# Optimization experiments

Hardware: AMD Instinct MI355X
Metric: run time of the kernel (lower is better)

The kernel has to match this reference:

```python
import jax, jax.numpy as jnp
import numpy as np

V_CNT = 10000
B = 16
N = B * V_CNT          # total nodes
K = 6                  # Chebyshev order
CH = [3, 128, 64, 32, 128]
G = 8                  # GroupNorm groups (divides 128, 64, 32)
EPS = 1e-5
AVG_DEG = 16


def setup_inputs() -> dict:
    key = jax.random.key(0)
    ks = jax.random.split(key, 8)
    n_edges = N * AVG_DEG
    inp = {
        "x": jax.random.normal(ks[0], (N, CH[0]), jnp.float32),
        "edge_index": jax.random.randint(ks[1], (2, n_edges), 0, N, jnp.int32).astype(jnp.int64),
    }
    for l in range(3):
        cin, cout = CH[l], CH[l + 1]
        s = (1.0 / (cin * K)) ** 0.5
        inp[f"W{l}"] = jax.random.uniform(ks[2 + l], (K, cin, cout), jnp.float32, -s, s)
        inp[f"b{l}"] = jnp.zeros((cout,), jnp.float32)
        inp[f"gamma{l}"] = jnp.ones((cout,), jnp.float32)
        inp[f"beta{l}"] = jnp.zeros((cout,), jnp.float32)
    din = V_CNT * CH[3]
    s = (1.0 / din) ** 0.5
    inp["W_last"] = jax.random.uniform(ks[5], (din, CH[4]), jnp.float32, -s, s)
    inp["b_last"] = jnp.zeros((CH[4],), jnp.float32)
    return inp


def _cheb_edge_weights(edge_index):
    # PyG ChebConv sym normalization with lambda_max=2: L_hat = L - I = -D^{-1/2} A D^{-1/2}
    row, col = edge_index[0], edge_index[1]
    deg = jax.ops.segment_sum(jnp.ones(row.shape, jnp.float32), row, num_segments=N)
    dis = jnp.where(deg > 0, jax.lax.rsqrt(jnp.maximum(deg, 1.0)), 0.0)  # deg^{-1/2}, inf->0
    return -dis[row] * dis[col], row, col


def _cheb_conv(x, row, col, w, W, b):
    # Chebyshev recursion: Tx0=x, Tx1=L_hat x, Tx_k = 2 L_hat Tx_{k-1} - Tx_{k-2}
    prop = lambda h: jax.ops.segment_sum(w[:, None] * h[col], row, num_segments=N)
    Tx0 = x
    out = Tx0 @ W[0]
    Tx1 = prop(Tx0)
    out = out + Tx1 @ W[1]
    for k in range(2, W.shape[0]):
        Tx2 = 2.0 * prop(Tx1) - Tx0
        out = out + Tx2 @ W[k]
        Tx0, Tx1 = Tx1, Tx2
    return out + b


def _group_norm(h, gamma, beta):
    n, C = h.shape
    hg = h.reshape(n, G, C // G)
    mu = hg.mean(axis=2, keepdims=True)
    var = hg.var(axis=2, keepdims=True)
    hg = (hg - mu) * jax.lax.rsqrt(var + EPS)
    return hg.reshape(n, C) * gamma + beta


def reference(x, edge_index, W0, b0, gamma0, beta0, W1, b1, gamma1, beta1,
              W2, b2, gamma2, beta2, W_last, b_last):
    w, row, col = _cheb_edge_weights(edge_index)
    Ws = [W0, W1, W2]
    bs = [b0, b1, b2]
    gs = [gamma0, gamma1, gamma2]
    betas = [beta0, beta1, beta2]
    h = x
    for l in range(3):
        h = _cheb_conv(h, row, col, w, Ws[l], bs[l])
        h = _group_norm(h, gs[l], betas[l])
        h = jax.nn.relu(h)
    h = h.reshape(-1, V_CNT * CH[3])  # [B, v_cnt*32]
    return h @ W_last + b_last
```

## Files before the change

### kernel.cpp

```cpp
#include <hip/hip_runtime.h>
#include <hip/hip_fp16.h>


#define NN 160000
#define EE 2560000
#define FD2 256
#define NBKT 625
#define BCAPL 13
#define ABLK 500
#define EPT 20

typedef __attribute__((ext_vector_type(8))) _Float16 half8;
typedef __attribute__((ext_vector_type(4))) float floatx4;

__device__ inline float2 h2f2(unsigned u) {
  __half2 h = __builtin_bit_cast(__half2, u);
  return __half22float2(h);
}
__device__ inline unsigned short f2h(float f) {
  return __builtin_bit_cast(unsigned short, __float2half_rn(f));
}
__device__ inline unsigned packh2(float a, float b) {
  return __builtin_bit_cast(unsigned, __floats2half2_rn(a, b));
}

__global__ __launch_bounds__(256) void k_binit(int* __restrict__ bcur) {
  int i = blockIdx.x * 256 + threadIdx.x;
  if (i < NBKT) bcur[i] = i << BCAPL;
}

__global__ __launch_bounds__(256) void k_bucketA(const int* __restrict__ ei,
                                                 int* __restrict__ bcur, unsigned* __restrict__ stg) {
  __shared__ int bcnt[NBKT];
  __shared__ int gbase[NBKT];
  int tid = threadIdx.x;
  for (int i = tid; i < NBKT; i += 256) bcnt[i] = 0;
  __syncthreads();
  int r[EPT];
  int e0 = blockIdx.x * (256 * EPT);
#pragma unroll
  for (int k = 0; k < EPT; k++) {
    int e = e0 + k * 256 + tid;
    r[k] = ei[e];
    atomicAdd(&bcnt[r[k] >> 8], 1);
  }
  __syncthreads();
  for (int i = tid; i < NBKT; i += 256) {
    gbase[i] = atomicAdd(&bcur[i], bcnt[i]);
    bcnt[i] = 0;
  }
  __syncthreads();
#pragma unroll
  for (int k = 0; k < EPT; k++) {
    int e = e0 + k * 256 + tid;
    int c = ei[EE + e];
    int b = r[k] >> 8;
    int off = atomicAdd(&bcnt[b], 1);
    int pos = gbase[b] + off;
    if (pos < ((b + 1) << BCAPL))
      stg[pos] = ((unsigned)(r[k] & 255) << 18) | (unsigned)c;
  }
}

__global__ void k_bktscan(const int* __restrict__ bcur, int* __restrict__ bbase,
                          int* __restrict__ rowStart) {
  __shared__ int s[1024];
  int tid = threadIdx.x;
  int tot = 0;
  if (tid < NBKT) {
    tot = bcur[tid] - (tid << BCAPL);
    if (tot > (1 << BCAPL)) tot = 1 << BCAPL;
  }
  s[tid] = tot;
  __syncthreads();
  for (int off = 1; off < 1024; off <<= 1) {
    int t = (tid >= off) ? s[tid - off] : 0;
    __syncthreads();
    s[tid] += t;
    __syncthreads();
  }
  if (tid < NBKT) bbase[tid] = s[tid] - tot;
  if (tid == 0) rowStart[NN] = EE;
}

__global__ __launch_bounds__(256) void k_bucketB1(const unsigned* __restrict__ stg, const int* __restrict__ bcur,
                                                  const int* __restrict__ bbase, int* __restrict__ rowStart,
                                                  float* __restrict__ dis) {
  __shared__ int degl[256];
  __shared__ int s[256];
  int b = blockIdx.x;
  int tid = threadIdx.x;
  degl[tid] = 0;
  __syncthreads();
  int cnt = bcur[b] - (b << BCAPL);
  if (cnt > (1 << BCAPL)) cnt = 1 << BCAPL;
  int base = b << BCAPL;
  for (int k = tid; k < cnt; k += 256)
    atomicAdd(&degl[stg[base + k] >> 18], 1);
  __syncthreads();
  int d = degl[tid];
  s[tid] = d;
  __syncthreads();
  for (int off = 1; off < 256; off <<= 1) {
    int t = (tid >= off) ? s[tid - off] : 0;
    __syncthreads();
    s[tid] += t;
    __syncthreads();
  }
  int r0 = b << 8;
  rowStart[r0 + tid] = bbase[b] + s[tid] - d;
  dis[r0 + tid] = d > 0 ? rsqrtf((float)d) : 0.f;
}

__global__ __launch_bounds__(256) void k_bucketB2(const unsigned* __restrict__ stg, const int* __restrict__ bcur,
                                                  const int* __restrict__ rowStart, const float* __restrict__ dis,
                                                  int2* __restrict__ ew) {
  __shared__ int curs[256];
  __shared__ float disl[256];
  int b = blockIdx.x;
  int tid = threadIdx.x;
  int r0 = b << 8;
  curs[tid] = rowStart[r0 + tid];
  disl[tid] = dis[r0 + tid];
  __syncthreads();
  int cnt = bcur[b] - (b << BCAPL);
  if (cnt > (1 << BCAPL)) cnt = 1 << BCAPL;
  int base = b << BCAPL;
  for (int k = tid; k < cnt; k += 256) {
    unsigned u = stg[base + k];
    int rlow = u >> 18;
    int c = u & 0x3FFFFu;
    int pos = atomicAdd(&curs[rlow], 1);
    float w = -disl[rlow] * dis[c];
    ew[pos] = make_int2(c, __float_as_int(w));
  }
}

__global__ __launch_bounds__(256) void k_copyx(const float* __restrict__ x, float* __restrict__ A,
                                               unsigned short* __restrict__ TxAll) {
  int i = blockIdx.x * 256 + threadIdx.x;
  if (i >= NN) return;
  float v0 = x[i * 3], v1 = x[i * 3 + 1], v2 = x[i * 3 + 2];
  A[i * 3] = v0; A[i * 3 + 1] = v1; A[i * 3 + 2] = v2;
  uint4* dst = reinterpret_cast<uint4*>(TxAll + (size_t)i * 32);
  uint4 z = make_uint4(0u, 0u, 0u, 0u);
  dst[0] = make_uint4(packh2(v0, v1), (unsigned)f2h(v2), 0u, 0u);
  dst[1] = z; dst[2] = z; dst[3] = z;
}

template <int MODE>
__global__ __launch_bounds__(256) void k_prop3(const float* __restrict__ Tsrc, float* __restrict__ Tdst,
                                               unsigned short* __restrict__ TxAll, int ks,
                                               const int* __restrict__ rowStart, const int2* __restrict__ ew) {
  int i = blockIdx.x * 256 + threadIdx.x;
  if (i >= NN) return;
  float a0 = 0.f, a1 = 0.f, a2 = 0.f;
  int e = rowStart[i], e1 = rowStart[i + 1];
  for (; e + 3 < e1; e += 4) {
    int2 p0 = ew[e], p1 = ew[e + 1], p2 = ew[e + 2], p3 = ew[e + 3];
    float w0 = __int_as_float(p0.y), w1 = __int_as_float(p1.y);
    float w2 = __int_as_float(p2.y), w3 = __int_as_float(p3.y);
    a0 += w0 * Tsrc[p0.x * 3] + w1 * Tsrc[p1.x * 3] + w2 * Tsrc[p2.x * 3] + w3 * Tsrc[p3.x * 3];
    a1 += w0 * Tsrc[p0.x * 3 + 1] + w1 * Tsrc[p1.x * 3 + 1] + w2 * Tsrc[p2.x * 3 + 1] + w3 * Tsrc[p3.x * 3 + 1];
    a2 += w0 * Tsrc[p0.x * 3 + 2] + w1 * Tsrc[p1.x * 3 + 2] + w2 * Tsrc[p2.x * 3 + 2] + w3 * Tsrc[p3.x * 3 + 2];
  }
  for (; e < e1; e++) {
    int2 p0 = ew[e];
    float w0 = __int_as_float(p0.y);
    a0 += w0 * Tsrc[p0.x * 3];
    a1 += w0 * Tsrc[p0.x * 3 + 1];
    a2 += w0 * Tsrc[p0.x * 3 + 2];
  }
  if (MODE == 2) {
    a0 = 2.f * a0 - Tdst[i * 3];
    a1 = 2.f * a1 - Tdst[i * 3 + 1];
    a2 = 2.f * a2 - Tdst[i * 3 + 2];
  }
  Tdst[i * 3] = a0; Tdst[i * 3 + 1] = a1; Tdst[i * 3 + 2] = a2;
  unsigned short* tp = TxAll + i * 32 + ks * 3;
  tp[0] = f2h(a0); tp[1] = f2h(a1); tp[2] = f2h(a2);
}

__global__ __launch_bounds__(256) void k_padW0(const float* __restrict__ W0, unsigned short* __restrict__ Bt) {
  int idx = blockIdx.x * 256 + threadIdx.x;
  if (idx >= 128 * 32) return;
  int co = idx >> 5, t = idx & 31;
  Bt[co * 32 + t] = (t < 18) ? f2h(W0[t * 128 + co]) : (unsigned short)0;
}

template <int CIN, int COUT>
__global__ __launch_bounds__(256) void k_combine(const float* __restrict__ W, unsigned short* __restrict__ Bt) {
  int idx = blockIdx.x * 256 + threadIdx.x;
  if (idx >= CIN * 6 * COUT) return;
  int co = idx % COUT;
  int j  = (idx / COUT) % 6;
  int ci = idx / (6 * COUT);
  float c0, c1, c2, c3, c4, c5;
  switch (j) {
    case 0:  c0 = 1;  c1 = 0;  c2 = -1; c3 = 0;   c4 = 1;  c5 = 0;   break;
    case 1:  c0 = 0;  c1 = 1;  c2 = 0;  c3 = -3;  c4 = 0;  c5 = 5;   break;
    case 2:  c0 = 0;  c1 = 0;  c2 = 2;  c3 = 0;   c4 = -8; c5 = 0;   break;
    case 3:  c0 = 0;  c1 = 0;  c2 = 0;  c3 = 4;   c4 = 0;  c5 = -20; break;
    case 4:  c0 = 0;  c1 = 0;  c2 = 0;  c3 = 0;   c4 = 8;  c5 = 0;   break;
    default: c0 = 0;  c1 = 0;  c2 = 0;  c3 = 0;   c4 = 0;  c5 = 16;  break;
  }
  float s = 0.f;
  s += c0 * W[(0 * CIN + ci) * COUT + co];
  s += c1 * W[(1 * CIN + ci) * COUT + co];
  s += c2 * W[(2 * CIN + ci) * COUT + co];
  s += c3 * W[(3 * CIN + ci) * COUT + co];
  s += c4 * W[(4 * CIN + ci) * COUT + co];
  s += c5 * W[(5 * CIN + ci) * COUT + co];
  Bt[(j * COUT + co) * CIN + ci] = f2h(s);
}

template <int KDIM, int COUT>
__global__ __launch_bounds__(256) void k_gemm(const unsigned short* __restrict__ A,
                                              const unsigned short* __restrict__ Bt,
                                              unsigned short* __restrict__ Y) {
  constexpr int KP = KDIM + 8;
  __shared__ unsigned short As[64 * KP];
  __shared__ unsigned short Bs[64 * KP];
  int i0 = blockIdx.x * 64;
  int c0 = blockIdx.y * 64;
  for (int idx = threadIdx.x; idx < 64 * (KDIM / 8); idx += 256) {
    int row = idx / (KDIM / 8), seg = idx % (KDIM / 8);
    uint4 v = ((const uint4*)A)[(size_t)(i0 + row) * (KDIM / 8) + seg];
    *reinterpret_cast<uint4*>(&As[row * KP + seg * 8]) = v;
  }
  for (int idx = threadIdx.x; idx < 64 * (KDIM / 8); idx += 256) {
    int row = idx / (KDIM / 8), seg = idx % (KDIM / 8);
    uint4 v = ((const uint4*)Bt)[(size_t)(c0 + row) * (KDIM / 8) + seg];
    *reinterpret_cast<uint4*>(&Bs[row * KP + seg * 8]) = v;
  }
  __syncthreads();
  int w = threadIdx.x >> 6, lane = threadIdx.x & 63;
  int mn = lane & 15, q = lane >> 4;
  floatx4 acc[4];
#pragma unroll
  for (int cb = 0; cb < 4; cb++) acc[cb] = {0.f, 0.f, 0.f, 0.f};
#pragma unroll
  for (int ks = 0; ks < KDIM / 32; ks++) {
    half8 af = *reinterpret_cast<const half8*>(&As[(16 * w + mn) * KP + ks * 32 + q * 8]);
#pragma unroll
    for (int cb = 0; cb < 4; cb++) {
      half8 bf = *reinterpret_cast<const half8*>(&Bs[(cb * 16 + mn) * KP + ks * 32 + q * 8]);
      acc[cb] = __builtin_amdgcn_mfma_f32_16x16x32_f16(af, bf, acc[cb], 0, 0, 0);
    }
  }
#pragma unroll
  for (int cb = 0; cb < 4; cb++) {
    int jc = c0 + cb * 16 + mn;
    int slice = jc / COUT, cc = jc % COUT;
    unsigned short* dst = Y + (size_t)slice * NN * COUT + cc;
#pragma unroll
    for (int r = 0; r < 4; r++) {
      int i = i0 + 16 * w + q * 4 + r;
      dst[(size_t)i * COUT] = f2h(acc[cb][r]);
    }
  }
}

template <int CPN>
__global__ __launch_bounds__(256) void k_horner(const unsigned* __restrict__ Ysrc, unsigned* __restrict__ Ydst,
                                                const int* __restrict__ rowStart, const int2* __restrict__ ew) {
  int t = blockIdx.x * 256 + threadIdx.x;
  int i = t / CPN;
  int cp = t % CPN;
  float2 a = h2f2(Ydst[(size_t)i * CPN + cp]);
  float acc0 = a.x, acc1 = a.y;
  int e = rowStart[i], e1 = rowStart[i + 1];
  for (; e + 7 < e1; e += 8) {
    int2 p[8];
    unsigned u[8];
#pragma unroll
    for (int k = 0; k < 8; k++) p[k] = ew[e + k];
#pragma unroll
    for (int k = 0; k < 8; k++) u[k] = Ysrc[(size_t)p[k].x * CPN + cp];
#pragma unroll
    for (int k = 0; k < 8; k++) {
      float w = __int_as_float(p[k].y);
      float2 f = h2f2(u[k]);
      acc0 += w * f.x;
      acc1 += w * f.y;
    }
  }
  for (; e < e1; e++) {
    int2 p0 = ew[e];
    float w0 = __int_as_float(p0.y);
    float2 f0 = h2f2(Ysrc[(size_t)p0.x * CPN + cp]);
    acc0 += w0 * f0.x;
    acc1 += w0 * f0.y;
  }
  Ydst[(size_t)i * CPN + cp] = packh2(acc0, acc1);
}

template <int CPG>
__global__ __launch_bounds__(256) void k_gn(const unsigned short* __restrict__ src, const float* __restrict__ bias,
                                            const float* __restrict__ gamma, const float* __restrict__ beta,
                                            unsigned short* __restrict__ dst) {
  constexpr int C = CPG * 8;
  int t = blockIdx.x * 256 + threadIdx.x;
  int i = t >> 3, g = t & 7;
  float v[CPG];
  const unsigned* p = reinterpret_cast<const unsigned*>(src + (size_t)i * C + g * CPG);
#pragma unroll
  for (int q = 0; q < CPG / 2; q++) {
    float2 f = h2f2(p[q]);
    v[2 * q] = f.x; v[2 * q + 1] = f.y;
  }
  float mean = 0.f;
#pragma unroll
  for (int c = 0; c < CPG; c++) { v[c] += bias[g * CPG + c]; mean += v[c]; }
  mean *= (1.f / CPG);
  float var = 0.f;
#pragma unroll
  for (int c = 0; c < CPG; c++) { float d = v[c] - mean; var += d * d; }
  var *= (1.f / CPG);
  float rs = rsqrtf(var + 1e-5f);
  unsigned* dp = reinterpret_cast<unsigned*>(dst + (size_t)i * C + g * CPG);
#pragma unroll
  for (int q = 0; q < CPG / 2; q++) {
    float o0 = fmaxf((v[2 * q] - mean) * rs * gamma[g * CPG + 2 * q] + beta[g * CPG + 2 * q], 0.f);
    float o1 = fmaxf((v[2 * q + 1] - mean) * rs * gamma[g * CPG + 2 * q + 1] + beta[g * CPG + 2 * q + 1], 0.f);
    dp[q] = packh2(o0, o1);
  }
}

__global__ __launch_bounds__(256) void k_final1(const unsigned short* __restrict__ h3,
                                                const float* __restrict__ Wl,
                                                float* __restrict__ part) {
  __shared__ float hs[16 * FD2];
  __shared__ float red[2048];
  int d0 = blockIdx.x * FD2;
  const unsigned* h3u = reinterpret_cast<const unsigned*>(h3);
  for (int idx = threadIdx.x; idx < 16 * (FD2 / 2); idx += 256) {
    int b = idx / (FD2 / 2), dq = idx % (FD2 / 2);
    float2 f = h2f2(h3u[(size_t)b * 160000 + (d0 >> 1) + dq]);
    hs[b * FD2 + 2 * dq] = f.x;
    hs[b * FD2 + 2 * dq + 1] = f.y;
  }
  __syncthreads();
  int w = threadIdx.x >> 6, lane = threadIdx.x & 63;
  float a0[16], a1[16];
#pragma unroll
  for (int b = 0; b < 16; b++) { a0[b] = 0.f; a1[b] = 0.f; }
  const float* wp = Wl + (size_t)(d0 + w * (FD2 / 4)) * 128 + 2 * lane;
#pragma unroll 2
  for (int r = 0; r < FD2 / 4; r++) {
    float2 wv = *reinterpret_cast<const float2*>(wp + (size_t)r * 128);
    int row = w * (FD2 / 4) + r;
#pragma unroll
    for (int b = 0; b < 16; b++) {
      float h = hs[b * FD2 + row];
      a0[b] += wv.x * h;
      a1[b] += wv.y * h;
    }
  }
  float2* red2 = reinterpret_cast<float2*>(red);
  for (int ww = 0; ww < 4; ww++) {
    if (w == ww) {
#pragma unroll
      for (int b = 0; b < 16; b++) {
        if (ww == 0) {
          red2[b * 64 + lane] = make_float2(a0[b], a1[b]);
        } else {
          float2 r2 = red2[b * 64 + lane];
          r2.x += a0[b]; r2.y += a1[b];
          red2[b * 64 + lane] = r2;
        }
      }
    }
    __syncthreads();
  }
  for (int i = threadIdx.x; i < 2048; i += 256)
    part[(size_t)blockIdx.x * 2048 + i] = red[i];
}

__global__ __launch_bounds__(256) void k_final2(const float* __restrict__ part, const float* __restrict__ bl,
                                                float* __restrict__ out) {
  int o = blockIdx.x * 256 + threadIdx.x;
  float s = bl[o & 127];
#pragma unroll 10
  for (int p = 0; p < 1250; p++) s += part[(size_t)p * 2048 + o];
  out[o] = s;
}

extern "C" void kernel_launch(void* const* d_in, const int* in_sizes, int n_in,
                              void* d_out, int out_size, void* d_ws, size_t ws_size,
                              hipStream_t stream) {
  const float* x   = (const float*)d_in[0];
  const int*   ei  = (const int*)d_in[1];
  const float* W0  = (const float*)d_in[2];
  const float* b0  = (const float*)d_in[3];
  const float* g0  = (const float*)d_in[4];
  const float* be0 = (const float*)d_in[5];
  const float* W1  = (const float*)d_in[6];
  const float* b1  = (const float*)d_in[7];
  const float* g1  = (const float*)d_in[8];
  const float* be1 = (const float*)d_in[9];
  const float* W2  = (const float*)d_in[10];
  const float* b2  = (const float*)d_in[11];
  const float* g2  = (const float*)d_in[12];
  const float* be2 = (const float*)d_in[13];
  const float* Wl  = (const float*)d_in[14];
  const float* bl  = (const float*)d_in[15];
  float* out = (float*)d_out;
  (void)in_sizes; (void)n_in; (void)out_size; (void)ws_size;

  char* pw = (char*)d_ws;
  auto carve = [&](size_t bytes) -> void* {
    void* r = (void*)pw;
    pw += (bytes + 255) & ~(size_t)255;
    return r;
  };
  int*            bcur     = (int*)   carve((size_t)NBKT * 4);
  int*            bbase    = (int*)   carve((size_t)NBKT * 4);
  int*            rowStart = (int*)   carve((size_t)(NN + 1) * 4);
  float*          dis      = (float*) carve((size_t)NN * 4);
  int2*           ew       = (int2*)  carve((size_t)EE * 8);
  unsigned short* Cwt      = (unsigned short*)carve((size_t)384 * 128 * 2);
  unsigned short* TxAll    = (unsigned short*)carve((size_t)NN * 32 * 2);
  float*          A3       = (float*) carve((size_t)NN * 3 * 4);
  float*          B3       = (float*) carve((size_t)NN * 3 * 4);
  unsigned short* Hbuf     = (unsigned short*)carve((size_t)NN * 128 * 2);
  unsigned short* Ybuf     = (unsigned short*)carve((size_t)NN * 384 * 2);
  float*          part     = (float*) carve((size_t)1250 * 2048 * 4);
  unsigned*       stg      = (unsigned*)Ybuf;

  k_binit<<<3, 256, 0, stream>>>(bcur);
  k_bucketA<<<ABLK, 256, 0, stream>>>(ei, bcur, stg);
  k_bktscan<<<1, 1024, 0, stream>>>(bcur, bbase, rowStart);
  k_bucketB1<<<NBKT, 256, 0, stream>>>(stg, bcur, bbase, rowStart, dis);
  k_bucketB2<<<NBKT, 256, 0, stream>>>(stg, bcur, rowStart, dis, ew);

  k_copyx<<<625, 256, 0, stream>>>(x, A3, TxAll);
  k_prop3<1><<<625, 256, 0, stream>>>(A3, B3, TxAll, 1, rowStart, ew);
  k_prop3<2><<<625, 256, 0, stream>>>(B3, A3, TxAll, 2, rowStart, ew);
  k_prop3<2><<<625, 256, 0, stream>>>(A3, B3, TxAll, 3, rowStart, ew);
  k_prop3<2><<<625, 256, 0, stream>>>(B3, A3, TxAll, 4, rowStart, ew);
  k_prop3<2><<<625, 256, 0, stream>>>(A3, B3, TxAll, 5, rowStart, ew);
  k_padW0<<<16, 256, 0, stream>>>(W0, Cwt);
  k_gemm<32, 128><<<dim3(2500, 2), 256, 0, stream>>>(TxAll, Cwt, Ybuf);
  k_gn<16><<<5000, 256, 0, stream>>>(Ybuf, b0, g0, be0, Hbuf);

  k_combine<128, 64><<<192, 256, 0, stream>>>(W1, Cwt);
  k_gemm<128, 64><<<dim3(2500, 6), 256, 0, stream>>>(Hbuf, Cwt, Ybuf);
  for (int j = 4; j >= 0; j--)
    k_horner<32><<<20000, 256, 0, stream>>>((unsigned*)(Ybuf + (size_t)(j + 1) * NN * 64),
                                            (unsigned*)(Ybuf + (size_t)j * NN * 64), rowStart, ew);
  k_gn<8><<<5000, 256, 0, stream>>>(Ybuf, b1, g1, be1, Hbuf);

  k_combine<64, 32><<<48, 256, 0, stream>>>(W2, Cwt);
  k_gemm<64, 32><<<dim3(2500, 3), 256, 0, stream>>>(Hbuf, Cwt, Ybuf);
  for (int j = 4; j >= 0; j--)
    k_horner<16><<<10000, 256, 0, stream>>>((unsigned*)(Ybuf + (size_t)(j + 1) * NN * 32),
                                            (unsigned*)(Ybuf + (size_t)j * NN * 32), rowStart, ew);
  k_gn<4><<<5000, 256, 0, stream>>>(Ybuf, b2, g2, be2, Hbuf);

  k_final1<<<1250, 256, 0, stream>>>(Hbuf, Wl, part);
  k_final2<<<8, 256, 0, stream>>>(part, bl, out);
}
```

Baseline: 1.281 ms.

## Fuse prep kernels, compress edge records, fuse GEMM/Horner with GroupNorm

Merges bucket init, weight combining/padding and x copy into one prep kernel, and folds the bucket scan into bucketB1 via a per-block reduction. Edge records shrink from 8-byte (col, weight) pairs to 4-byte words packing column and neighbour degree, with the weight rebuilt by rsqrt on the fly and the row-side scale applied once per node. The layer-0 GEMM now applies bias, GroupNorm and ReLU in its epilogue, and the last Horner step of layers 1 and 2 does the same, removing the separate GN passes. The aim is fewer launches and less gather traffic. The cost is extra rsqrt work per edge and degrees clamped to 8191.

```diff
diff --git a/kernel.cpp b/kernel.cpp
--- a/kernel.cpp
+++ b/kernel.cpp
@@ -24,174 +24,8 @@
   return __builtin_bit_cast(unsigned, __floats2half2_rn(a, b));
 }
 
-__global__ __launch_bounds__(256) void k_binit(int* __restrict__ bcur) {
-  int i = blockIdx.x * 256 + threadIdx.x;
-  if (i < NBKT) bcur[i] = i << BCAPL;
-}
-
-__global__ __launch_bounds__(256) void k_bucketA(const int* __restrict__ ei,
-                                                 int* __restrict__ bcur, unsigned* __restrict__ stg) {
-  __shared__ int bcnt[NBKT];
-  __shared__ int gbase[NBKT];
-  int tid = threadIdx.x;
-  for (int i = tid; i < NBKT; i += 256) bcnt[i] = 0;
-  __syncthreads();
-  int r[EPT];
-  int e0 = blockIdx.x * (256 * EPT);
-#pragma unroll
-  for (int k = 0; k < EPT; k++) {
-    int e = e0 + k * 256 + tid;
-    r[k] = ei[e];
-    atomicAdd(&bcnt[r[k] >> 8], 1);
-  }
-  __syncthreads();
-  for (int i = tid; i < NBKT; i += 256) {
-    gbase[i] = atomicAdd(&bcur[i], bcnt[i]);
-    bcnt[i] = 0;
-  }
-  __syncthreads();
-#pragma unroll
-  for (int k = 0; k < EPT; k++) {
-    int e = e0 + k * 256 + tid;
-    int c = ei[EE + e];
-    int b = r[k] >> 8;
-    int off = atomicAdd(&bcnt[b], 1);
-    int pos = gbase[b] + off;
-    if (pos < ((b + 1) << BCAPL))
-      stg[pos] = ((unsigned)(r[k] & 255) << 18) | (unsigned)c;
-  }
-}
-
-__global__ void k_bktscan(const int* __restrict__ bcur, int* __restrict__ bbase,
-                          int* __restrict__ rowStart) {
-  __shared__ int s[1024];
-  int tid = threadIdx.x;
-  int tot = 0;
-  if (tid < NBKT) {
-    tot = bcur[tid] - (tid << BCAPL);
-    if (tot > (1 << BCAPL)) tot = 1 << BCAPL;
-  }
-  s[tid] = tot;
-  __syncthreads();
-  for (int off = 1; off < 1024; off <<= 1) {
-    int t = (tid >= off) ? s[tid - off] : 0;
-    __syncthreads();
-    s[tid] += t;
-    __syncthreads();
-  }
-  if (tid < NBKT) bbase[tid] = s[tid] - tot;
-  if (tid == 0) rowStart[NN] = EE;
-}
-
-__global__ __launch_bounds__(256) void k_bucketB1(const unsigned* __restrict__ stg, const int* __restrict__ bcur,
-                                                  const int* __restrict__ bbase, int* __restrict__ rowStart,
-                                                  float* __restrict__ dis) {
-  __shared__ int degl[256];
-  __shared__ int s[256];
-  int b = blockIdx.x;
-  int tid = threadIdx.x;
-  degl[tid] = 0;
-  __syncthreads();
-  int cnt = bcur[b] - (b << BCAPL);
-  if (cnt > (1 << BCAPL)) cnt = 1 << BCAPL;
-  int base = b << BCAPL;
-  for (int k = tid; k < cnt; k += 256)
-    atomicAdd(&degl[stg[base + k] >> 18], 1);
-  __syncthreads();
-  int d = degl[tid];
-  s[tid] = d;
-  __syncthreads();
-  for (int off = 1; off < 256; off <<= 1) {
-    int t = (tid >= off) ? s[tid - off] : 0;
-    __syncthreads();
-    s[tid] += t;
-    __syncthreads();
-  }
-  int r0 = b << 8;
-  rowStart[r0 + tid] = bbase[b] + s[tid] - d;
-  dis[r0 + tid] = d > 0 ? rsqrtf((float)d) : 0.f;
-}
-
-__global__ __launch_bounds__(256) void k_bucketB2(const unsigned* __restrict__ stg, const int* __restrict__ bcur,
-                                                  const int* __restrict__ rowStart, const float* __restrict__ dis,
-                                                  int2* __restrict__ ew) {
-  __shared__ int curs[256];
-  __shared__ float disl[256];
-  int b = blockIdx.x;
-  int tid = threadIdx.x;
-  int r0 = b << 8;
-  curs[tid] = rowStart[r0 + tid];
-  disl[tid] = dis[r0 + tid];
-  __syncthreads();
-  int cnt = bcur[b] - (b << BCAPL);
-  if (cnt > (1 << BCAPL)) cnt = 1 << BCAPL;
-  int base = b << BCAPL;
-  for (int k = tid; k < cnt; k += 256) {
-    unsigned u = stg[base + k];
-    int rlow = u >> 18;
-    int c = u & 0x3FFFFu;
-    int pos = atomicAdd(&curs[rlow], 1);
-    float w = -disl[rlow] * dis[c];
-    ew[pos] = make_int2(c, __float_as_int(w));
-  }
-}
-
-__global__ __launch_bounds__(256) void k_copyx(const float* __restrict__ x, float* __restrict__ A,
-                                               unsigned short* __restrict__ TxAll) {
-  int i = blockIdx.x * 256 + threadIdx.x;
-  if (i >= NN) return;
-  float v0 = x[i * 3], v1 = x[i * 3 + 1], v2 = x[i * 3 + 2];
-  A[i * 3] = v0; A[i * 3 + 1] = v1; A[i * 3 + 2] = v2;
-  uint4* dst = reinterpret_cast<uint4*>(TxAll + (size_t)i * 32);
-  uint4 z = make_uint4(0u, 0u, 0u, 0u);
-  dst[0] = make_uint4(packh2(v0, v1), (unsigned)f2h(v2), 0u, 0u);
-  dst[1] = z; dst[2] = z; dst[3] = z;
-}
-
-template <int MODE>
-__global__ __launch_bounds__(256) void k_prop3(const float* __restrict__ Tsrc, float* __restrict__ Tdst,
-                                               unsigned short* __restrict__ TxAll, int ks,
-                                               const int* __restrict__ rowStart, const int2* __restrict__ ew) {
-  int i = blockIdx.x * 256 + threadIdx.x;
-  if (i >= NN) return;
-  float a0 = 0.f, a1 = 0.f, a2 = 0.f;
-  int e = rowStart[i], e1 = rowStart[i + 1];
-  for (; e + 3 < e1; e += 4) {
-    int2 p0 = ew[e], p1 = ew[e + 1], p2 = ew[e + 2], p3 = ew[e + 3];
-    float w0 = __int_as_float(p0.y), w1 = __int_as_float(p1.y);
-    float w2 = __int_as_float(p2.y), w3 = __int_as_float(p3.y);
-    a0 += w0 * Tsrc[p0.x * 3] + w1 * Tsrc[p1.x * 3] + w2 * Tsrc[p2.x * 3] + w3 * Tsrc[p3.x * 3];
-    a1 += w0 * Tsrc[p0.x * 3 + 1] + w1 * Tsrc[p1.x * 3 + 1] + w2 * Tsrc[p2.x * 3 + 1] + w3 * Tsrc[p3.x * 3 + 1];
-    a2 += w0 * Tsrc[p0.x * 3 + 2] + w1 * Tsrc[p1.x * 3 + 2] + w2 * Tsrc[p2.x * 3 + 2] + w3 * Tsrc[p3.x * 3 + 2];
-  }
-  for (; e < e1; e++) {
-    int2 p0 = ew[e];
-    float w0 = __int_as_float(p0.y);
-    a0 += w0 * Tsrc[p0.x * 3];
-    a1 += w0 * Tsrc[p0.x * 3 + 1];
-    a2 += w0 * Tsrc[p0.x * 3 + 2];
-  }
-  if (MODE == 2) {
-    a0 = 2.f * a0 - Tdst[i * 3];
-    a1 = 2.f * a1 - Tdst[i * 3 + 1];
-    a2 = 2.f * a2 - Tdst[i * 3 + 2];
-  }
-  Tdst[i * 3] = a0; Tdst[i * 3 + 1] = a1; Tdst[i * 3 + 2] = a2;
-  unsigned short* tp = TxAll + i * 32 + ks * 3;
-  tp[0] = f2h(a0); tp[1] = f2h(a1); tp[2] = f2h(a2);
-}
-
-__global__ __launch_bounds__(256) void k_padW0(const float* __restrict__ W0, unsigned short* __restrict__ Bt) {
-  int idx = blockIdx.x * 256 + threadIdx.x;
-  if (idx >= 128 * 32) return;
-  int co = idx >> 5, t = idx & 31;
-  Bt[co * 32 + t] = (t < 18) ? f2h(W0[t * 128 + co]) : (unsigned short)0;
-}
-
 template <int CIN, int COUT>
-__global__ __launch_bounds__(256) void k_combine(const float* __restrict__ W, unsigned short* __restrict__ Bt) {
-  int idx = blockIdx.x * 256 + threadIdx.x;
-  if (idx >= CIN * 6 * COUT) return;
+__device__ inline void combine_item(const float* __restrict__ W, unsigned short* __restrict__ Bt, int idx) {
   int co = idx % COUT;
   int j  = (idx / COUT) % 6;
   int ci = idx / (6 * COUT);
@@ -212,6 +46,240 @@
   s += c4 * W[(4 * CIN + ci) * COUT + co];
   s += c5 * W[(5 * CIN + ci) * COUT + co];
   Bt[(j * COUT + co) * CIN + ci] = f2h(s);
+}
+
+__global__ __launch_bounds__(256) void k_prep(const float* __restrict__ W0, const float* __restrict__ W1,
+                                              const float* __restrict__ W2, const float* __restrict__ x,
+                                              int* __restrict__ bcur, unsigned short* __restrict__ Cwt0,
+                                              unsigned short* __restrict__ Cwt1, unsigned short* __restrict__ Cwt2,
+                                              float* __restrict__ A3, unsigned short* __restrict__ TxAll) {
+  int idx = blockIdx.x * 256 + threadIdx.x;
+  if (idx < NBKT) { bcur[idx] = idx << BCAPL; return; }
+  idx -= NBKT;
+  if (idx < 128 * 32) {
+    int co = idx >> 5, t = idx & 31;
+    Cwt0[co * 32 + t] = (t < 18) ? f2h(W0[t * 128 + co]) : (unsigned short)0;
+    return;
+  }
+  idx -= 128 * 32;
+  if (idx < 128 * 6 * 64) { combine_item<128, 64>(W1, Cwt1, idx); return; }
+  idx -= 128 * 6 * 64;
+  if (idx < 64 * 6 * 32) { combine_item<64, 32>(W2, Cwt2, idx); return; }
+  idx -= 64 * 6 * 32;
+  if (idx < NN) {
+    int i = idx;
+    float v0 = x[i * 3], v1 = x[i * 3 + 1], v2 = x[i * 3 + 2];
+    A3[i * 3] = v0; A3[i * 3 + 1] = v1; A3[i * 3 + 2] = v2;
+    uint4* dst = reinterpret_cast<uint4*>(TxAll + (size_t)i * 32);
+    uint4 z = make_uint4(0u, 0u, 0u, 0u);
+    dst[0] = make_uint4(packh2(v0, v1), (unsigned)f2h(v2), 0u, 0u);
+    dst[1] = z; dst[2] = z; dst[3] = z;
+  }
+}
+
+__global__ __launch_bounds__(256) void k_bucketA(const int* __restrict__ ei,
+                                                 int* __restrict__ bcur, unsigned* __restrict__ stg) {
+  __shared__ int bcnt[NBKT];
+  __shared__ int gbase[NBKT];
+  int tid = threadIdx.x;
+  for (int i = tid; i < NBKT; i += 256) bcnt[i] = 0;
+  __syncthreads();
+  int r[EPT];
+  int e0 = blockIdx.x * (256 * EPT);
+#pragma unroll
+  for (int k = 0; k < EPT; k++) {
+    int e = e0 + k * 256 + tid;
+    r[k] = ei[e];
+    atomicAdd(&bcnt[r[k] >> 8], 1);
+  }
+  __syncthreads();
+  for (int i = tid; i < NBKT; i += 256) {
+    gbase[i] = atomicAdd(&bcur[i], bcnt[i]);
+    bcnt[i] = 0;
+  }
+  __syncthreads();
+#pragma unroll
+  for (int k = 0; k < EPT; k++) {
+    int e = e0 + k * 256 + tid;
+    int c = ei[EE + e];
+    int b = r[k] >> 8;
+    int off = atomicAdd(&bcnt[b], 1);
+    int pos = gbase[b] + off;
+    if (pos < ((b + 1) << BCAPL))
+      stg[pos] = ((unsigned)(r[k] & 255) << 18) | (unsigned)c;
+  }
+}
+
+__global__ __launch_bounds__(256) void k_bucketB1(const unsigned* __restrict__ stg, const int* __restrict__ bcur,
+                                                  int* __restrict__ rowStart, float* __restrict__ dis,
+                                                  int* __restrict__ deg) {
+  __shared__ int degl[256];
+  __shared__ int s[256];
+  __shared__ int red[256];
+  int b = blockIdx.x;
+  int tid = threadIdx.x;
+  int part = 0;
+  for (int j = tid; j < NBKT; j += 256) {
+    int cj = bcur[j] - (j << BCAPL);
+    if (cj > (1 << BCAPL)) cj = 1 << BCAPL;
+    if (j < b) part += cj;
+  }
+  red[tid] = part;
+  degl[tid] = 0;
+  __syncthreads();
+  for (int off = 128; off > 0; off >>= 1) {
+    if (tid < off) red[tid] += red[tid + off];
+    __syncthreads();
+  }
+  int bbase = red[0];
+  int cnt = bcur[b] - (b << BCAPL);
+  if (cnt > (1 << BCAPL)) cnt = 1 << BCAPL;
+  int base = b << BCAPL;
+  for (int k = tid; k < cnt; k += 256)
+    atomicAdd(&degl[stg[base + k] >> 18], 1);
+  __syncthreads();
+  int d = degl[tid];
+  s[tid] = d;
+  __syncthreads();
+  for (int off = 1; off < 256; off <<= 1) {
+    int t = (tid >= off) ? s[tid - off] : 0;
+    __syncthreads();
+    s[tid] += t;
+    __syncthreads();
+  }
+  int r0 = b << 8;
+  rowStart[r0 + tid] = bbase + s[tid] - d;
+  dis[r0 + tid] = d > 0 ? rsqrtf((float)d) : 0.f;
+  deg[r0 + tid] = d;
+  if (b == 0 && tid == 0) rowStart[NN] = EE;
+}
+
+__global__ __launch_bounds__(256) void k_bucketB2(const unsigned* __restrict__ stg, const int* __restrict__ bcur,
+                                                  const int* __restrict__ rowStart, const int* __restrict__ deg,
+                                                  unsigned* __restrict__ ewc) {
+  __shared__ int curs[256];
+  int b = blockIdx.x;
+  int tid = threadIdx.x;
+  int r0 = b << 8;
+  curs[tid] = rowStart[r0 + tid];
+  __syncthreads();
+  int cnt = bcur[b] - (b << BCAPL);
+  if (cnt > (1 << BCAPL)) cnt = 1 << BCAPL;
+  int base = b << BCAPL;
+  for (int k = tid; k < cnt; k += 256) {
+    unsigned u = stg[base + k];
+    int rlow = u >> 18;
+    int c = u & 0x3FFFFu;
+    int pos = atomicAdd(&curs[rlow], 1);
+    int dc = deg[c];
+    if (dc > 8191) dc = 8191;
+    ewc[pos] = (unsigned)c | ((unsigned)dc << 18);
+  }
+}
+
+template <int MODE>
+__global__ __launch_bounds__(256) void k_prop3(const float* __restrict__ Tsrc, float* __restrict__ Tdst,
+                                               unsigned short* __restrict__ TxAll, int ks,
+                                               const int* __restrict__ rowStart, const unsigned* __restrict__ ewc,
+                                               const float* __restrict__ dis) {
+  int i = blockIdx.x * 256 + threadIdx.x;
+  if (i >= NN) return;
+  float s0 = 0.f, s1 = 0.f, s2 = 0.f;
+  int e = rowStart[i], e1 = rowStart[i + 1];
+  for (; e + 3 < e1; e += 4) {
+    unsigned u0 = ewc[e], u1 = ewc[e + 1], u2 = ewc[e + 2], u3 = ewc[e + 3];
+    int c0 = u0 & 0x3FFFFu, c1 = u1 & 0x3FFFFu, c2 = u2 & 0x3FFFFu, c3 = u3 & 0x3FFFFu;
+    unsigned d0 = u0 >> 18, d1 = u1 >> 18, d2 = u2 >> 18, d3 = u3 >> 18;
+    float w0 = d0 ? rsqrtf((float)d0) : 0.f;
+    float w1 = d1 ? rsqrtf((float)d1) : 0.f;
+    float w2 = d2 ? rsqrtf((float)d2) : 0.f;
+    float w3 = d3 ? rsqrtf((float)d3) : 0.f;
+    s0 += w0 * Tsrc[c0 * 3] + w1 * Tsrc[c1 * 3] + w2 * Tsrc[c2 * 3] + w3 * Tsrc[c3 * 3];
+    s1 += w0 * Tsrc[c0 * 3 + 1] + w1 * Tsrc[c1 * 3 + 1] + w2 * Tsrc[c2 * 3 + 1] + w3 * Tsrc[c3 * 3 + 1];
+    s2 += w0 * Tsrc[c0 * 3 + 2] + w1 * Tsrc[c1 * 3 + 2] + w2 * Tsrc[c2 * 3 + 2] + w3 * Tsrc[c3 * 3 + 2];
+  }
+  for (; e < e1; e++) {
+    unsigned u0 = ewc[e];
+    int c0 = u0 & 0x3FFFFu;
+    unsigned d0 = u0 >> 18;
+    float w0 = d0 ? rsqrtf((float)d0) : 0.f;
+    s0 += w0 * Tsrc[c0 * 3];
+    s1 += w0 * Tsrc[c0 * 3 + 1];
+    s2 += w0 * Tsrc[c0 * 3 + 2];
+  }
+  float ndr = -dis[i];
+  float a0 = ndr * s0, a1 = ndr * s1, a2 = ndr * s2;
+  if (MODE == 2) {
+    a0 = 2.f * a0 - Tdst[i * 3];
+    a1 = 2.f * a1 - Tdst[i * 3 + 1];
+    a2 = 2.f * a2 - Tdst[i * 3 + 2];
+  }
+  Tdst[i * 3] = a0; Tdst[i * 3 + 1] = a1; Tdst[i * 3 + 2] = a2;
+  unsigned short* tp = TxAll + i * 32 + ks * 3;
+  tp[0] = f2h(a0); tp[1] = f2h(a1); tp[2] = f2h(a2);
+}
+
+__global__ __launch_bounds__(256) void k_gemm0gn(const unsigned short* __restrict__ A,
+                                                 const unsigned short* __restrict__ Bt,
+                                                 const float* __restrict__ bias, const float* __restrict__ gamma,
+                                                 const float* __restrict__ beta, unsigned short* __restrict__ H) {
+  constexpr int KP = 40;
+  __shared__ unsigned short As[64 * KP];
+  __shared__ unsigned short Bs[128 * KP];
+  __shared__ float pb[128], pg[128], pe[128];
+  int i0 = blockIdx.x * 64;
+  for (int idx = threadIdx.x; idx < 64 * 4; idx += 256) {
+    int row = idx >> 2, seg = idx & 3;
+    uint4 v = ((const uint4*)A)[(size_t)(i0 + row) * 4 + seg];
+    *reinterpret_cast<uint4*>(&As[row * KP + seg * 8]) = v;
+  }
+  for (int idx = threadIdx.x; idx < 128 * 4; idx += 256) {
+    int row = idx >> 2, seg = idx & 3;
+    uint4 v = ((const uint4*)Bt)[(size_t)row * 4 + seg];
+    *reinterpret_cast<uint4*>(&Bs[row * KP + seg * 8]) = v;
+  }
+  if (threadIdx.x < 128) {
+    pb[threadIdx.x] = bias[threadIdx.x];
+    pg[threadIdx.x] = gamma[threadIdx.x];
+    pe[threadIdx.x] = beta[threadIdx.x];
+  }
+  __syncthreads();
+  int w = threadIdx.x >> 6, lane = threadIdx.x & 63;
+  int mn = lane & 15, q = lane >> 4;
+  floatx4 acc[8];
+#pragma unroll
+  for (int cb = 0; cb < 8; cb++) acc[cb] = {0.f, 0.f, 0.f, 0.f};
+  half8 af = *reinterpret_cast<const half8*>(&As[(16 * w + mn) * KP + q * 8]);
+#pragma unroll
+  for (int cb = 0; cb < 8; cb++) {
+    half8 bf = *reinterpret_cast<const half8*>(&Bs[(cb * 16 + mn) * KP + q * 8]);
+    acc[cb] = __builtin_amdgcn_mfma_f32_16x16x32_f16(af, bf, acc[cb], 0, 0, 0);
+  }
+#pragma unroll
+  for (int cb = 0; cb < 8; cb++) {
+    int ch = cb * 16 + mn;
+    float bs = pb[ch], ga = pg[ch], be = pe[ch];
+    float v[4], S[4];
+#pragma unroll
+    for (int r = 0; r < 4; r++) { v[r] = acc[cb][r] + bs; S[r] = v[r]; }
+#pragma unroll
+    for (int m = 1; m < 16; m <<= 1)
+#pragma unroll
+      for (int r = 0; r < 4; r++) S[r] += __shfl_xor(S[r], m);
+    float d[4], Q[4];
+#pragma unroll
+    for (int r = 0; r < 4; r++) { d[r] = v[r] - S[r] * 0.0625f; Q[r] = d[r] * d[r]; }
+#pragma unroll
+    for (int m = 1; m < 16; m <<= 1)
+#pragma unroll
+      for (int r = 0; r < 4; r++) Q[r] += __shfl_xor(Q[r], m);
+#pragma unroll
+    for (int r = 0; r < 4; r++) {
+      float rs = rsqrtf(Q[r] * 0.0625f + 1e-5f);
+      int i = i0 + 16 * w + q * 4 + r;
+      H[(size_t)i * 128 + ch] = f2h(fmaxf(d[r] * rs * ga + be, 0.f));
+    }
+  }
 }
 
 template <int KDIM, int COUT>
@@ -261,69 +329,66 @@
   }
 }
 
-template <int CPN>
+template <int CPN, int FUSE>
 __global__ __launch_bounds__(256) void k_horner(const unsigned* __restrict__ Ysrc, unsigned* __restrict__ Ydst,
-                                                const int* __restrict__ rowStart, const int2* __restrict__ ew) {
+                                                const int* __restrict__ rowStart, const unsigned* __restrict__ ewc,
+                                                const float* __restrict__ dis, unsigned* __restrict__ dst,
+                                                const float* __restrict__ bias, const float* __restrict__ gamma,
+                                                const float* __restrict__ beta) {
   int t = blockIdx.x * 256 + threadIdx.x;
   int i = t / CPN;
   int cp = t % CPN;
   float2 a = h2f2(Ydst[(size_t)i * CPN + cp]);
-  float acc0 = a.x, acc1 = a.y;
+  float s0 = 0.f, s1 = 0.f;
   int e = rowStart[i], e1 = rowStart[i + 1];
   for (; e + 7 < e1; e += 8) {
-    int2 p[8];
-    unsigned u[8];
-#pragma unroll
-    for (int k = 0; k < 8; k++) p[k] = ew[e + k];
-#pragma unroll
-    for (int k = 0; k < 8; k++) u[k] = Ysrc[(size_t)p[k].x * CPN + cp];
+    unsigned uu[8], u[8];
+    float wv[8];
+#pragma unroll
+    for (int k = 0; k < 8; k++) uu[k] = ewc[e + k];
+#pragma unroll
+    for (int k = 0; k < 8; k++) u[k] = Ysrc[(size_t)(uu[k] & 0x3FFFFu) * CPN + cp];
 #pragma unroll
     for (int k = 0; k < 8; k++) {
-      float w = __int_as_float(p[k].y);
+      unsigned dc = uu[k] >> 18;
+      wv[k] = dc ? rsqrtf((float)dc) : 0.f;
+    }
+#pragma unroll
+    for (int k = 0; k < 8; k++) {
       float2 f = h2f2(u[k]);
-      acc0 += w * f.x;
-      acc1 += w * f.y;
+      s0 += wv[k] * f.x;
+      s1 += wv[k] * f.y;
     }
   }
   for (; e < e1; e++) {
-    int2 p0 = ew[e];
-    float w0 = __int_as_float(p0.y);
-    float2 f0 = h2f2(Ysrc[(size_t)p0.x * CPN + cp]);
-    acc0 += w0 * f0.x;
-    acc1 += w0 * f0.y;
-  }
-  Ydst[(size_t)i * CPN + cp] = packh2(acc0, acc1);
-}
-
-template <int CPG>
-__global__ __launch_bounds__(256) void k_gn(const unsigned short* __restrict__ src, const float* __restrict__ bias,
-                                            const float* __restrict__ gamma, const float* __restrict__ beta,
-                                            unsigned short* __restrict__ dst) {
-  constexpr int C = CPG * 8;
-  int t = blockIdx.x * 256 + threadIdx.x;
-  int i = t >> 3, g = t & 7;
-  float v[CPG];
-  const unsigned* p = reinterpret_cast<const unsigned*>(src + (size_t)i * C + g * CPG);
-#pragma unroll
-  for (int q = 0; q < CPG / 2; q++) {
-    float2 f = h2f2(p[q]);
-    v[2 * q] = f.x; v[2 * q + 1] = f.y;
-  }
-  float mean = 0.f;
-#pragma unroll
-  for (int c = 0; c < CPG; c++) { v[c] += bias[g * CPG + c]; mean += v[c]; }
-  mean *= (1.f / CPG);
-  float var = 0.f;
-#pragma unroll
-  for (int c = 0; c < CPG; c++) { float d = v[c] - mean; var += d * d; }
-  var *= (1.f / CPG);
-  float rs = rsqrtf(var + 1e-5f);
-  unsigned* dp = reinterpret_cast<unsigned*>(dst + (size_t)i * C + g * CPG);
-#pragma unroll
-  for (int q = 0; q < CPG / 2; q++) {
-    float o0 = fmaxf((v[2 * q] - mean) * rs * gamma[g * CPG + 2 * q] + beta[g * CPG + 2 * q], 0.f);
-    float o1 = fmaxf((v[2 * q + 1] - mean) * rs * gamma[g * CPG + 2 * q + 1] + beta[g * CPG + 2 * q + 1], 0.f);
-    dp[q] = packh2(o0, o1);
+    unsigned u0 = ewc[e];
+    unsigned dc = u0 >> 18;
+    float w0 = dc ? rsqrtf((float)dc) : 0.f;
+    float2 f0 = h2f2(Ysrc[(size_t)(u0 & 0x3FFFFu) * CPN + cp]);
+    s0 += w0 * f0.x;
+    s1 += w0 * f0.y;
+  }
+  float ndr = -dis[i];
+  float v0 = a.x + ndr * s0, v1 = a.y + ndr * s1;
+  if (FUSE == 0) {
+    Ydst[(size_t)i * CPN + cp] = packh2(v0, v1);
+  } else {
+    constexpr int CPG = CPN / 4;
+    constexpr int LPG = CPN / 8;
+    v0 += bias[2 * cp];
+    v1 += bias[2 * cp + 1];
+    float s = v0 + v1;
+#pragma unroll
+    for (int m = 1; m < LPG; m <<= 1) s += __shfl_xor(s, m);
+    float mean = s * (1.0f / CPG);
+    float d0 = v0 - mean, d1 = v1 - mean;
+    float qq = d0 * d0 + d1 * d1;
+#pragma unroll
+    for (int m = 1; m < LPG; m <<= 1) qq += __shfl_xor(qq, m);
+    float rs = rsqrtf(qq * (1.0f / CPG) + 1e-5f);
+    float o0 = fmaxf(d0 * rs * gamma[2 * cp] + beta[2 * cp], 0.f);
+    float o1 = fmaxf(d1 * rs * gamma[2 * cp + 1] + beta[2 * cp + 1], 0.f);
+    dst[(size_t)i * CPN + cp] = packh2(o0, o1);
   }
 }
 
@@ -415,11 +480,13 @@
     return r;
   };
   int*            bcur     = (int*)   carve((size_t)NBKT * 4);
-  int*            bbase    = (int*)   carve((size_t)NBKT * 4);
   int*            rowStart = (int*)   carve((size_t)(NN + 1) * 4);
   float*          dis      = (float*) carve((size_t)NN * 4);
-  int2*           ew       = (int2*)  carve((size_t)EE * 8);
-  unsigned short* Cwt      = (unsigned short*)carve((size_t)384 * 128 * 2);
+  int*            deg      = (int*)   carve((size_t)NN * 4);
+  unsigned*       ewc      = (unsigned*)carve((size_t)EE * 4);
+  unsigned short* Cwt0     = (unsigned short*)carve((size_t)128 * 32 * 2);
+  unsigned short* Cwt1     = (unsigned short*)carve((size_t)384 * 128 * 2);
+  unsigned short* Cwt2     = (unsigned short*)carve((size_t)192 * 64 * 2);
   unsigned short* TxAll    = (unsigned short*)carve((size_t)NN * 32 * 2);
   float*          A3       = (float*) carve((size_t)NN * 3 * 4);
   float*          B3       = (float*) carve((size_t)NN * 3 * 4);
@@ -428,35 +495,35 @@
   float*          part     = (float*) carve((size_t)1250 * 2048 * 4);
   unsigned*       stg      = (unsigned*)Ybuf;
 
-  k_binit<<<3, 256, 0, stream>>>(bcur);
+  k_prep<<<884, 256, 0, stream>>>(W0, W1, W2, x, bcur, Cwt0, Cwt1, Cwt2, A3, TxAll);
   k_bucketA<<<ABLK, 256, 0, stream>>>(ei, bcur, stg);
-  k_bktscan<<<1, 1024, 0, stream>>>(bcur, bbase, rowStart);
-  k_bucketB1<<<NBKT, 256, 0, stream>>>(stg, bcur, bbase, rowStart, dis);
-  k_bucketB2<<<NBKT, 256, 0, stream>>>(stg, bcur, rowStart, dis, ew);
-
-  k_copyx<<<625, 256, 0, stream>>>(x, A3, TxAll);
-  k_prop3<1><<<625, 256, 0, stream>>>(A3, B3, TxAll, 1, rowStart, ew);
-  k_prop3<2><<<625, 256, 0, stream>>>(B3, A3, TxAll, 2, rowStart, ew);
-  k_prop3<2><<<625, 256, 0, stream>>>(A3, B3, TxAll, 3, rowStart, ew);
-  k_prop3<2><<<625, 256, 0, stream>>>(B3, A3, TxAll, 4, rowStart, ew);
-  k_prop3<2><<<625, 256, 0, stream>>>(A3, B3, TxAll, 5, rowStart, ew);
-  k_padW0<<<16, 256, 0, stream>>>(W0, Cwt);
-  k_gemm<32, 128><<<dim3(2500, 2), 256, 0, stream>>>(TxAll, Cwt, Ybuf);
-  k_gn<16><<<5000, 256, 0, stream>>>(Ybuf, b0, g0, be0, Hbuf);
-
-  k_combine<128, 64><<<192, 256, 0, stream>>>(W1, Cwt);
-  k_gemm<128, 64><<<dim3(2500, 6), 256, 0, stream>>>(Hbuf, Cwt, Ybuf);
-  for (int j = 4; j >= 0; j--)
-    k_horner<32><<<20000, 256, 0, stream>>>((unsigned*)(Ybuf + (size_t)(j + 1) * NN * 64),
-                                            (unsigned*)(Ybuf + (size_t)j * NN * 64), rowStart, ew);
-  k_gn<8><<<5000, 256, 0, stream>>>(Ybuf, b1, g1, be1, Hbuf);
-
-  k_combine<64, 32><<<48, 256, 0, stream>>>(W2, Cwt);
-  k_gemm<64, 32><<<dim3(2500, 3), 256, 0, stream>>>(Hbuf, Cwt, Ybuf);
-  for (int j = 4; j >= 0; j--)
-    k_horner<16><<<10000, 256, 0, stream>>>((unsigned*)(Ybuf + (size_t)(j + 1) * NN * 32),
-                                            (unsigned*)(Ybuf + (size_t)j * NN * 32), rowStart, ew);
-  k_gn<4><<<5000, 256, 0, stream>>>(Ybuf, b2, g2, be2, Hbuf);
+  k_bucketB1<<<NBKT, 256, 0, stream>>>(stg, bcur, rowStart, dis, deg);
+  k_bucketB2<<<NBKT, 256, 0, stream>>>(stg, bcur, rowStart, deg, ewc);
+
+  k_prop3<1><<<625, 256, 0, stream>>>(A3, B3, TxAll, 1, rowStart, ewc, dis);
+  k_prop3<2><<<625, 256, 0, stream>>>(B3, A3, TxAll, 2, rowStart, ewc, dis);
+  k_prop3<2><<<625, 256, 0, stream>>>(A3, B3, TxAll, 3, rowStart, ewc, dis);
+  k_prop3<2><<<625, 256, 0, stream>>>(B3, A3, TxAll, 4, rowStart, ewc, dis);
+  k_prop3<2><<<625, 256, 0, stream>>>(A3, B3, TxAll, 5, rowStart, ewc, dis);
+  k_gemm0gn<<<2500, 256, 0, stream>>>(TxAll, Cwt0, b0, g0, be0, Hbuf);
+
+  k_gemm<128, 64><<<dim3(2500, 6), 256, 0, stream>>>(Hbuf, Cwt1, Ybuf);
+  for (int j = 4; j >= 1; j--)
+    k_horner<32, 0><<<20000, 256, 0, stream>>>((unsigned*)(Ybuf + (size_t)(j + 1) * NN * 64),
+                                               (unsigned*)(Ybuf + (size_t)j * NN * 64), rowStart, ewc, dis,
+                                               nullptr, nullptr, nullptr, nullptr);
+  k_horner<32, 1><<<20000, 256, 0, stream>>>((unsigned*)(Ybuf + (size_t)NN * 64),
+                                             (unsigned*)Ybuf, rowStart, ewc, dis,
+                                             (unsigned*)Hbuf, b1, g1, be1);
+
+  k_gemm<64, 32><<<dim3(2500, 3), 256, 0, stream>>>(Hbuf, Cwt2, Ybuf);
+  for (int j = 4; j >= 1; j--)
+    k_horner<16, 0><<<10000, 256, 0, stream>>>((unsigned*)(Ybuf + (size_t)(j + 1) * NN * 32),
+                                               (unsigned*)(Ybuf + (size_t)j * NN * 32), rowStart, ewc, dis,
+                                               nullptr, nullptr, nullptr, nullptr);
+  k_horner<16, 1><<<10000, 256, 0, stream>>>((unsigned*)(Ybuf + (size_t)NN * 32),
+                                             (unsigned*)Ybuf, rowStart, ewc, dis,
+                                             (unsigned*)Hbuf, b2, g2, be2);
 
   k_final1<<<1250, 256, 0, stream>>>(Hbuf, Wl, part);
   k_final2<<<8, 256, 0, stream>>>(part, bl, out);
```

Result: faster. 1.223 ms (-4.5%).
